# Kernel optimization log

Measured on AMD Instinct MI355X. Metric: run time of the kernel, lower is better.

## Reference

```python
import jax, jax.numpy as jnp
import numpy as np

B_IMG = 2
N_PROP = 2000
N_GT = 16
C_FEAT = 256
H_FEAT = 128
W_FEAT = 128
IMG = 1024.0
NUM_CLASSES = 2
BG_THRESH = 0.5          # fg==bg==0.5 -> BETWEEN_THRESHOLDS band is empty
BPI = 512                # batch_size_per_image
NUM_POS_MAX = int(BPI * 0.25)
ENC_W = (1.0, 1.0, 1.0, 1.0, 1.0)
SCALE = 1.0 / 8.0        # feature stride
POOL = 7
SR = 2                   # sampling_ratio
BETA = 1.0 / 9.0
HID = 1024


def _make_boxes(key, shape_prefix, img=IMG):
    kc, ks = jax.random.split(key)
    c = jax.random.uniform(kc, shape_prefix + (2,), minval=0.0, maxval=img)
    s = jax.random.uniform(ks, shape_prefix + (2,), minval=20.0, maxval=200.0)
    lo = jnp.clip(c - 0.5 * s, 0.0, img - 2.0)
    hi = jnp.clip(c + 0.5 * s, lo + 1.0, img)
    return jnp.concatenate([lo, hi], axis=-1)  # [.., x1,y1,x2,y2]


def setup_inputs():
    key = jax.random.key(0)
    ks = jax.random.split(key, 12)
    features = jax.random.normal(ks[0], (B_IMG, C_FEAT, H_FEAT, W_FEAT), dtype=jnp.float32)
    proposals = _make_boxes(ks[1], (B_IMG, N_PROP))
    gt_boxes = _make_boxes(ks[2], (B_IMG, N_GT))
    gt_labels = jax.random.randint(ks[3], (B_IMG, N_GT), 1, NUM_CLASSES, dtype=jnp.int32)
    ka, kb, kt = jax.random.split(ks[4], 3)
    a = jax.random.uniform(ka, (B_IMG, N_GT), minval=10.0, maxval=60.0)
    b = jax.random.uniform(kb, (B_IMG, N_GT), minval=5.0, maxval=30.0)
    th = jax.random.uniform(kt, (B_IMG, N_GT), minval=-np.pi / 2, maxval=np.pi / 2)
    exy = 0.5 * (gt_boxes[..., :2] + gt_boxes[..., 2:])
    gt_ellipses = jnp.stack([a, b, exy[..., 0], exy[..., 1], th], axis=-1)
    d_in = C_FEAT * POOL * POOL
    w1 = jax.random.normal(ks[5], (d_in, HID), dtype=jnp.float32) * 0.02
    b1 = jnp.zeros((HID,), jnp.float32)
    w2 = jax.random.normal(ks[6], (HID, HID), dtype=jnp.float32) * 0.02
    b2 = jnp.zeros((HID,), jnp.float32)
    wc = jax.random.normal(ks[7], (HID, NUM_CLASSES), dtype=jnp.float32) * 0.02
    bc = jnp.zeros((NUM_CLASSES,), jnp.float32)
    wr = jax.random.normal(ks[8], (HID, NUM_CLASSES * 6), dtype=jnp.float32) * 0.02
    br = jnp.zeros((NUM_CLASSES * 6,), jnp.float32)
    return dict(features=features, proposals=proposals, gt_boxes=gt_boxes,
                gt_labels=gt_labels, gt_ellipses=gt_ellipses,
                w1=w1, b1=b1, w2=w2, b2=b2, wc=wc, bc=bc, wr=wr, br=br)


def box_iou(b1, b2):  # [G,4], [P,4] -> [G,P]
    a1 = (b1[:, 2] - b1[:, 0]) * (b1[:, 3] - b1[:, 1])
    a2 = (b2[:, 2] - b2[:, 0]) * (b2[:, 3] - b2[:, 1])
    lt = jnp.maximum(b1[:, None, :2], b2[None, :, :2])
    rb = jnp.minimum(b1[:, None, 2:], b2[None, :, 2:])
    wh = jnp.clip(rb - lt, 0.0)
    inter = wh[..., 0] * wh[..., 1]
    return inter / (a1[:, None] + a2[None, :] - inter)


def encode_ellipses(ell, boxes):  # ell [..,5]=(a,b,cx,cy,theta), boxes [..,4] -> [..,6]
    a, b, ex, ey, th = (ell[..., i] for i in range(5))
    w = jnp.maximum(boxes[..., 2] - boxes[..., 0], 1.0)
    h = jnp.maximum(boxes[..., 3] - boxes[..., 1], 1.0)
    cx = 0.5 * (boxes[..., 0] + boxes[..., 2])
    cy = 0.5 * (boxes[..., 1] + boxes[..., 3])
    wx, wy, wa, wb, wt = ENC_W
    dx = wx * (ex - cx) / w
    dy = wy * (ey - cy) / h
    da = wa * jnp.log(jnp.maximum(2.0 * a, 1e-3) / w)
    db = wb * jnp.log(jnp.maximum(2.0 * b, 1e-3) / h)
    return jnp.stack([dx, dy, da, db, wt * jnp.sin(2.0 * th), wt * jnp.cos(2.0 * th)], axis=-1)


def roi_align(fmap, rois):  # [C,H,W], [R,4] -> [R,C,POOL,POOL]
    C, H, W = fmap.shape
    r = rois * SCALE
    x1, y1, x2, y2 = r[:, 0], r[:, 1], r[:, 2], r[:, 3]
    bw = jnp.maximum(x2 - x1, 1.0) / POOL
    bh = jnp.maximum(y2 - y1, 1.0) / POOL
    S = POOL * SR
    off = (jnp.arange(S, dtype=jnp.float32) + 0.5) / SR  # bin-unit sample offsets
    ys = jnp.clip(y1[:, None] + off[None, :] * bh[:, None], 0.0, H - 1.0)  # [R,S]
    xs = jnp.clip(x1[:, None] + off[None, :] * bw[:, None], 0.0, W - 1.0)
    y0 = jnp.clip(jnp.floor(ys), 0, H - 2).astype(jnp.int32)
    x0 = jnp.clip(jnp.floor(xs), 0, W - 2).astype(jnp.int32)
    ly = ys - y0
    lx = xs - x0
    Ya, Yb = y0[:, :, None], (y0 + 1)[:, :, None]  # [R,S,1]
    Xa, Xb = x0[:, None, :], (x0 + 1)[:, None, :]  # [R,1,S]
    v00 = fmap[:, Ya, Xa]; v01 = fmap[:, Ya, Xb]   # [C,R,S,S]
    v10 = fmap[:, Yb, Xa]; v11 = fmap[:, Yb, Xb]
    wy1 = ly[:, :, None]; wy0 = 1.0 - wy1
    wx1 = lx[:, None, :]; wx0 = 1.0 - wx1
    val = v00 * (wy0 * wx0) + v01 * (wy0 * wx1) + v10 * (wy1 * wx0) + v11 * (wy1 * wx1)
    R = rois.shape[0]
    pooled = val.reshape(C, R, POOL, SR, POOL, SR).mean(axis=(3, 5))
    return pooled.transpose(1, 0, 2, 3)


def reference(features, proposals, gt_boxes, gt_labels, gt_ellipses,
              w1, b1, w2, b2, wc, bc, wr, br):
    B = features.shape[0]
    # add_gt_proposals
    props = jnp.concatenate([proposals, gt_boxes], axis=1)            # [B,P,4]
    # assign_targets_to_proposals: IoU + Matcher (fg=bg=0.5)
    iou = jax.vmap(box_iou)(gt_boxes, props)                          # [B,G,P]
    matched_vals = iou.max(axis=1)
    matches = iou.argmax(axis=1)                                      # [B,P]
    lab = jnp.take_along_axis(gt_labels, matches, axis=1)
    lab = jnp.where(matched_vals < BG_THRESH, 0, lab)                 # background
    # BalancedPositiveNegativeSampler (deterministic, fixed-shape):
    # cap positives at NUM_POS_MAX by random rank, fill rest with random negatives
    rand = jax.random.uniform(jax.random.key(42), lab.shape)
    is_pos = lab > 0
    is_neg = lab == 0
    pos_s = jnp.where(is_pos, rand, -1e9)
    rank = jnp.argsort(jnp.argsort(-pos_s, axis=1), axis=1)
    capped = is_pos & (rank < NUM_POS_MAX)
    prio = jnp.where(capped, rand + 2.0, jnp.where(is_neg, rand, -1e9))
    _, idx = jax.lax.top_k(prio, BPI)                                 # [B,512]
    boxes = jnp.take_along_axis(props, idx[..., None], axis=1)        # [B,512,4]
    labels = jnp.take_along_axis(lab, idx, axis=1)                    # [B,512]
    m = jnp.take_along_axis(matches, idx, axis=1)
    ell = jnp.take_along_axis(gt_ellipses, m[..., None], axis=1)      # [B,512,5]
    targets = encode_ellipses(ell, boxes)                             # [B,512,6]
    # RoIAlign + TwoMLPHead + predictor
    pooled = jax.vmap(roi_align)(features, boxes)                     # [B,512,C,7,7]
    N = B * BPI
    x = pooled.reshape(N, -1)
    x = jax.nn.relu(x @ w1 + b1)
    x = jax.nn.relu(x @ w2 + b2)
    logits = x @ wc + bc                                              # [N,2]
    reg = (x @ wr + br).reshape(N, NUM_CLASSES, 6)
    # ellipse_rcnn_loss
    labels_f = labels.reshape(N)
    t = targets.reshape(N, 6)
    ce = -jnp.take_along_axis(jax.nn.log_softmax(logits, axis=-1), labels_f[:, None], axis=1).mean()
    pred = jnp.take_along_axis(reg, labels_f[:, None, None], axis=1)[:, 0]  # [N,6]
    d = jnp.abs(pred - t)
    sl1 = jnp.where(d < BETA, 0.5 * d * d / BETA, d - 0.5 * BETA)
    reg_loss = jnp.sum(sl1 * (labels_f > 0)[:, None].astype(sl1.dtype)) / N
    return jnp.stack([ce, reg_loss])
```

## Files before the change

kernel.cpp:

```cpp
#include <hip/hip_runtime.h>
#include <hip/hip_bf16.h>
#include <math.h>

#define B_IMG   2
#define N_PROP  2000
#define N_GT    16
#define NPROPS  2016
#define C_FEAT  256
#define H_FEAT  128
#define W_FEAT  128
#define HWF     (H_FEAT*W_FEAT)
#define POOL    7
#define BPI     512
#define NPOSMAX 128
#define NSEL    (B_IMG*BPI)
#define K1      (C_FEAT*POOL*POOL)
#define K1P     12800
#define HID     1024
#define NHEAD   14
#define SPLITK1 8
#define G1_KC   1600

typedef short bf16x8f __attribute__((ext_vector_type(8)));
typedef float f32x4f  __attribute__((ext_vector_type(4)));
typedef short short4v __attribute__((ext_vector_type(4)));

__device__ __forceinline__ void threefry2x32(unsigned k0, unsigned k1,
                                             unsigned& x0, unsigned& x1) {
  unsigned ks[3] = {k0, k1, k0 ^ k1 ^ 0x1BD11BDAu};
  const int R0[4] = {13, 15, 26, 6};
  const int R1[4] = {17, 29, 16, 24};
  x0 += ks[0]; x1 += ks[1];
#pragma unroll
  for (int g = 0; g < 5; g++) {
    const int* rot = (g & 1) ? R1 : R0;
#pragma unroll
    for (int r = 0; r < 4; r++) {
      x0 += x1;
      x1 = (x1 << rot[r]) | (x1 >> (32 - rot[r]));
      x1 ^= x0;
    }
    x0 += ks[(g + 1) % 3];
    x1 += ks[(g + 2) % 3] + (unsigned)(g + 1);
  }
}

#define PRE_SAMPLE   2
#define PRE_TRANS    (PRE_SAMPLE + 2048)
#define PRE_CAST1    (PRE_TRANS + 3136)
#define PRE_CAST0    (PRE_CAST1 + 256)
#define PRE_TOTAL    (PRE_CAST0 + 512)

__global__ __launch_bounds__(256) void k_pre(const float* __restrict__ proposals,
                                             const float* __restrict__ gt_boxes,
                                             const int* __restrict__ gt_labels,
                                             const float* __restrict__ features,
                                             const float* __restrict__ w1,
                                             const float* __restrict__ w2,
                                             const float* __restrict__ gt_ell,
                                             __hip_bfloat16* __restrict__ featT,
                                             __hip_bfloat16* __restrict__ W1T,
                                             __hip_bfloat16* __restrict__ W2T,
                                             __hip_bfloat16* __restrict__ Xb,
                                             float* __restrict__ sel_boxes,
                                             int* __restrict__ sel_labels,
                                             float* __restrict__ targets) {
  __shared__ __align__(16) char smem[16640];
  int bid = blockIdx.x;
  int tid = threadIdx.x;
  if (bid < PRE_SAMPLE) {
    float* rs           = (float*)smem;
    unsigned char* mtl  = (unsigned char*)(smem + 8064);
    short* pos_i        = (short*)(smem + 10080);
    short* glist        = (short*)(smem + 10080);
    int*   Hs           = (int*)(smem + 14112);
    int*   curs         = (int*)(smem + 15140);
    float* gtb          = (float*)(smem + 16176);
    int*   gtl          = (int*)(smem + 16432);
    int*   cnt          = (int*)(smem + 16496);
    int b = bid;
    int base = b * NPROPS;
    if (tid == 0) *cnt = 0;
    if (tid < N_GT * 4) gtb[tid] = gt_boxes[b * N_GT * 4 + tid];
    if (tid < N_GT) gtl[tid] = gt_labels[b * N_GT + tid];
    __syncthreads();

    auto emitsel = [&](int slot, int i, int lab) {
      float p0, p1, p2, p3;
      if (i < N_PROP) {
        const float4 v = *(const float4*)(proposals + ((size_t)b * N_PROP + i) * 4);
        p0 = v.x; p1 = v.y; p2 = v.z; p3 = v.w;
      } else {
        const float* g = &gtb[(i - N_PROP) * 4];
        p0 = g[0]; p1 = g[1]; p2 = g[2]; p3 = g[3];
      }
      sel_boxes[slot * 4 + 0] = p0;
      sel_boxes[slot * 4 + 1] = p1;
      sel_boxes[slot * 4 + 2] = p2;
      sel_boxes[slot * 4 + 3] = p3;
      sel_labels[slot] = lab;
      int m = mtl[i] & 15;
      const float* e = gt_ell + ((size_t)b * N_GT + m) * 5;
      float ea = e[0], eb = e[1], ex = e[2], ey = e[3], eth = e[4];
      float w = fmaxf(p2 - p0, 1.0f), h = fmaxf(p3 - p1, 1.0f);
      float cx = 0.5f * (p0 + p2), cy = 0.5f * (p1 + p3);
      float* t = targets + (size_t)slot * 6;
      t[0] = (ex - cx) / w;
      t[1] = (ey - cy) / h;
      t[2] = logf(fmaxf(2.0f * ea, 0.001f) / w);
      t[3] = logf(fmaxf(2.0f * eb, 0.001f) / h);
      t[4] = sinf(2.0f * eth);
      t[5] = cosf(2.0f * eth);
    };

    for (int i = tid; i < NPROPS; i += 256) {
      unsigned x0 = 0u, x1 = (unsigned)(base + i);
      threefry2x32(0u, 42u, x0, x1);
      unsigned bits = x0 ^ x1;
      float r = __uint_as_float((bits >> 9) | 0x3F800000u) - 1.0f;
      rs[i] = r;
      float p0, p1, p2, p3;
      if (i < N_PROP) {
        const float4 v = *(const float4*)(proposals + ((size_t)b * N_PROP + i) * 4);
        p0 = v.x; p1 = v.y; p2 = v.z; p3 = v.w;
      } else {
        const float* g = &gtb[(i - N_PROP) * 4];
        p0 = g[0]; p1 = g[1]; p2 = g[2]; p3 = g[3];
      }
      float a2 = (p2 - p0) * (p3 - p1);
      float best = -1.0f; int bg = 0;
#pragma unroll
      for (int g = 0; g < N_GT; g++) {
        float g0 = gtb[g*4], g1 = gtb[g*4+1], g2 = gtb[g*4+2], g3 = gtb[g*4+3];
        float a1 = (g2 - g0) * (g3 - g1);
        float wx = fmaxf(fminf(g2, p2) - fmaxf(g0, p0), 0.0f);
        float wy = fmaxf(fminf(g3, p3) - fmaxf(g1, p1), 0.0f);
        float inter = wx * wy;
        float iou = inter / (a1 + a2 - inter);
        if (iou > best) { best = iou; bg = g; }
      }
      int lab = (best < 0.5f) ? 0 : gtl[bg];
      mtl[i] = (unsigned char)(bg | (lab ? 16 : 0));
      if (lab > 0) {
        int s = atomicAdd(cnt, 1);
        pos_i[s] = (short)i;
      }
    }
    __syncthreads();
    int P = *cnt;
    int Pp = (P < NPOSMAX) ? P : NPOSMAX;
    for (int s = tid; s < P; s += 256) {
      int i = pos_i[s]; float ri = rs[i];
      int ch = 0;
      for (int j = 0; j < P; j++) {
        int ij = pos_i[j]; float rj = rs[ij];
        ch += (rj > ri || (rj == ri && ij < i)) ? 1 : 0;
      }
      if (ch < NPOSMAX) {
        int m16 = mtl[i] & 15;
        int lab = gtl[m16];
        emitsel(b * BPI + ch, i, lab);
      }
    }
    __syncthreads();
    for (int idx = tid; idx < 257; idx += 256) Hs[idx] = 0;
    curs[tid] = 0;
    __syncthreads();
    for (int i = tid; i < NPROPS; i += 256)
      if (!(mtl[i] & 16)) {
        int bin = (int)(rs[i] * 256.0f); if (bin > 255) bin = 255;
        atomicAdd(&Hs[bin], 1);
      }
    __syncthreads();
    for (int off = 1; off < 256; off <<= 1) {
      int v = Hs[tid] + ((tid + off <= 256) ? Hs[tid + off] : 0);
      __syncthreads();
      Hs[tid] = v;
      __syncthreads();
    }
    for (int i = tid; i < NPROPS; i += 256)
      if (!(mtl[i] & 16)) {
        int bin = (int)(rs[i] * 256.0f); if (bin > 255) bin = 255;
        int o = atomicAdd(&curs[bin], 1);
        glist[Hs[bin + 1] + o] = (short)i;
      }
    __syncthreads();
    for (int i = tid; i < NPROPS; i += 256)
      if (!(mtl[i] & 16)) {
        int bin = (int)(rs[i] * 256.0f); if (bin > 255) bin = 255;
        int bbase = Hs[bin + 1];
        int cntb = Hs[bin] - bbase;
        float ri = rs[i];
        int wr = 0;
        for (int t = 0; t < cntb; t++) {
          int j = glist[bbase + t];
          if (j != i) {
            float rj = rs[j];
            wr += (rj > ri || (rj == ri && j < i)) ? 1 : 0;
          }
        }
        int slot = Pp + bbase + wr;
        if (slot < BPI) emitsel(b * BPI + slot, i, 0);
      }
  } else if (bid < PRE_TRANS) {
    float (*tile)[65] = (float(*)[65])smem;
    int t = bid - PRE_SAMPLE;
    int b = t >> 10;
    int rem = t & 1023;
    int c0 = (rem >> 8) * 64;
    int s0 = (rem & 255) * 64;
    const float* src = features + (size_t)b * C_FEAT * HWF;
    __hip_bfloat16* dst = featT + (size_t)b * HWF * C_FEAT;
    int hw4 = (tid & 15) * 4, cr = tid >> 4;
#pragma unroll
    for (int p = 0; p < 4; p++) {
      int c = cr + p * 16;
      float4 v = *(const float4*)(src + (size_t)(c0 + c) * HWF + s0 + hw4);
      tile[hw4 + 0][c] = v.x; tile[hw4 + 1][c] = v.y;
      tile[hw4 + 2][c] = v.z; tile[hw4 + 3][c] = v.w;
    }
    __syncthreads();
    int c4 = (tid & 15) * 4, hr = tid >> 4;
#pragma unroll
    for (int p = 0; p < 4; p++) {
      int hw = hr + p * 16;
      __hip_bfloat16 o[4] = {__float2bfloat16(tile[hw][c4]), __float2bfloat16(tile[hw][c4+1]),
                             __float2bfloat16(tile[hw][c4+2]), __float2bfloat16(tile[hw][c4+3])};
      *(short4v*)(dst + (size_t)(s0 + hw) * C_FEAT + c0 + c4) = *(short4v*)o;
    }
  } else if (bid < PRE_CAST1) {
    float (*tile)[65] = (float(*)[65])smem;
    int t = bid - PRE_TRANS;
    int p = t >> 6;
    int rem = t & 63;
    int c0 = (rem & 3) * 64;
    int n0 = (rem >> 2) * 64;
    int n4 = (tid & 15) * 4, ig = tid >> 4;
#pragma unroll
    for (int i = ig; i < 64; i += 16) {
      float4 v = *(const float4*)(w1 + (size_t)((c0 + i) * 49 + p) * HID + n0 + n4);
      tile[i][n4] = v.x; tile[i][n4 + 1] = v.y;
      tile[i][n4 + 2] = v.z; tile[i][n4 + 3] = v.w;
    }
    __syncthreads();
    int c4 = (tid & 15) * 4;
#pragma unroll
    for (int i = ig; i < 64; i += 16) {
      __hip_bfloat16 o[4] = {__float2bfloat16(tile[c4][i]), __float2bfloat16(tile[c4 + 1][i]),
                             __float2bfloat16(tile[c4 + 2][i]), __float2bfloat16(tile[c4 + 3][i])};
      *(short4v*)(W1T + (size_t)(n0 + i) * K1P + p * 256 + c0 + c4) = *(short4v*)o;
    }
  } else if (bid < PRE_CAST0) {
    float (*tile)[65] = (float(*)[65])smem;
    int t = bid - PRE_CAST1;
    int c0 = (t & 15) * 64;
    int n0 = (t >> 4) * 64;
    int n4 = (tid & 15) * 4, ig = tid >> 4;
#pragma unroll
    for (int i = ig; i < 64; i += 16) {
      float4 v = *(const float4*)(w2 + (size_t)(c0 + i) * HID + n0 + n4);
      tile[i][n4] = v.x; tile[i][n4 + 1] = v.y;
      tile[i][n4 + 2] = v.z; tile[i][n4 + 3] = v.w;
    }
    __syncthreads();
    int c4 = (tid & 15) * 4;
#pragma unroll
    for (int i = ig; i < 64; i += 16) {
      __hip_bfloat16 o[4] = {__float2bfloat16(tile[c4][i]), __float2bfloat16(tile[c4 + 1][i]),
                             __float2bfloat16(tile[c4 + 2][i]), __float2bfloat16(tile[c4 + 3][i])};
      *(short4v*)(W2T + (size_t)(n0 + i) * HID + c0 + c4) = *(short4v*)o;
    }
  } else {
    int t = bid - PRE_CAST0;
    __hip_bfloat16* buf = (t >> 8) ? W1T : Xb;
    int tt = (t & 255) * 256 + tid;
    int row = tt >> 6;
    int col4 = (tt & 63) << 2;
    short4v z = {0, 0, 0, 0};
    *(short4v*)(buf + (size_t)row * K1P + K1 + col4) = z;
  }
}

__global__ __launch_bounds__(256) void k_roialign(const __hip_bfloat16* __restrict__ featT,
                                                  const float* __restrict__ sel_boxes,
                                                  __hip_bfloat16* __restrict__ X) {
  int n = blockIdx.x;
  int py = blockIdx.y;
  int t = threadIdx.x;
  int px = t >> 5;
  int lane32 = t & 31;
  int c = lane32 << 3;
  int b = n >> 9;
  const float* bx = sel_boxes + (size_t)n * 4;
  float x1 = bx[0] * 0.125f, y1 = bx[1] * 0.125f;
  float x2 = bx[2] * 0.125f, y2 = bx[3] * 0.125f;
  float bw = fmaxf(x2 - x1, 1.0f) / 7.0f;
  float bh = fmaxf(y2 - y1, 1.0f) / 7.0f;
  if (px >= 7) return;
  const __hip_bfloat16* base = featT + (size_t)b * HWF * C_FEAT;
  int y0A[2]; float lyA[2];
#pragma unroll
  for (int sy = 0; sy < 2; sy++) {
    float off = ((float)(py * 2 + sy) + 0.5f) * 0.5f;
    float ys = fminf(fmaxf(y1 + off * bh, 0.0f), 127.0f);
    int y0 = (int)fminf(fmaxf(floorf(ys), 0.0f), 126.0f);
    y0A[sy] = y0; lyA[sy] = ys - (float)y0;
  }
  float acc[8] = {};
#pragma unroll
  for (int sx = 0; sx < 2; sx++) {
    float off = ((float)(px * 2 + sx) + 0.5f) * 0.5f;
    float xs = fminf(fmaxf(x1 + off * bw, 0.0f), 127.0f);
    int x0 = (int)fminf(fmaxf(floorf(xs), 0.0f), 126.0f);
    float lx = xs - (float)x0;
#pragma unroll
    for (int sy = 0; sy < 2; sy++) {
      int y0 = y0A[sy]; float ly = lyA[sy];
      const __hip_bfloat16* p = base + ((size_t)(y0 * W_FEAT + x0)) * C_FEAT + c;
      bf16x8f s00 = *(const bf16x8f*)p;
      bf16x8f s01 = *(const bf16x8f*)(p + C_FEAT);
      bf16x8f s10 = *(const bf16x8f*)(p + W_FEAT * C_FEAT);
      bf16x8f s11 = *(const bf16x8f*)(p + W_FEAT * C_FEAT + C_FEAT);
      float w00 = (1.0f - ly) * (1.0f - lx), w01 = (1.0f - ly) * lx;
      float w10 = ly * (1.0f - lx), w11 = ly * lx;
#pragma unroll
      for (int q = 0; q < 8; q++) {
        float v00 = __uint_as_float(((unsigned)(unsigned short)s00[q]) << 16);
        float v01 = __uint_as_float(((unsigned)(unsigned short)s01[q]) << 16);
        float v10 = __uint_as_float(((unsigned)(unsigned short)s10[q]) << 16);
        float v11 = __uint_as_float(((unsigned)(unsigned short)s11[q]) << 16);
        acc[q] += v00 * w00 + v01 * w01 + v10 * w10 + v11 * w11;
      }
    }
  }
  __hip_bfloat16 o[8];
#pragma unroll
  for (int q = 0; q < 8; q++) o[q] = __float2bfloat16(acc[q] * 0.25f);
  *(bf16x8f*)&X[(size_t)n * K1P + (size_t)(py * 7 + px) * C_FEAT + c] = *(bf16x8f*)o;
}

__device__ __forceinline__ void gld_lds16(const __hip_bfloat16* g, __hip_bfloat16* l) {
  __builtin_amdgcn_global_load_lds(
      (const __attribute__((address_space(1))) void*)g,
      (__attribute__((address_space(3))) void*)l, 16, 0, 0);
}

__global__ __launch_bounds__(256) void k_gemm1s(const __hip_bfloat16* __restrict__ A,
                                                const __hip_bfloat16* __restrict__ BT,
                                                __hip_bfloat16* __restrict__ Pb) {
  __shared__ __align__(16) __hip_bfloat16 As[128 * 32];
  __shared__ __align__(16) __hip_bfloat16 Bs[128 * 32];
  int lin = blockIdx.x;
  int kz = lin & 7;
  int q  = lin >> 3;
  int n0 = (q & 7) * 128;
  int m0 = (q >> 3) * 128;
  int tid = threadIdx.x;
  int kbeg = kz * G1_KC;
  int srow = tid >> 2;
  int scs  = tid & 3;
  int sg   = scs ^ (srow & 3);
  int scol = sg << 3;
  int wave = tid >> 6, lane = tid & 63;
  int wm = (wave & 1) * 64, wn = (wave >> 1) * 64;
  int lm = lane & 15, quad = lane >> 4;
  int fco = ((quad ^ (lm & 3)) << 3);
  f32x4f acc[4][4] = {};
  for (int k0 = kbeg; k0 < kbeg + G1_KC; k0 += 32) {
    __syncthreads();
#pragma unroll
    for (int r0 = 0; r0 < 128; r0 += 64)
      gld_lds16(A + (size_t)(m0 + r0 + srow) * K1P + k0 + scol, &As[(r0 + srow) * 32 + scs * 8]);
#pragma unroll
    for (int r0 = 0; r0 < 128; r0 += 64)
      gld_lds16(BT + (size_t)(n0 + r0 + srow) * K1P + k0 + scol, &Bs[(r0 + srow) * 32 + scs * 8]);
    __syncthreads();
    bf16x8f af[4], bf[4];
#pragma unroll
    for (int i = 0; i < 4; i++)
      af[i] = *(const bf16x8f*)&As[(wm + i * 16 + lm) * 32 + fco];
#pragma unroll
    for (int j = 0; j < 4; j++)
      bf[j] = *(const bf16x8f*)&Bs[(wn + j * 16 + lm) * 32 + fco];
#pragma unroll
    for (int i = 0; i < 4; i++)
#pragma unroll
      for (int j = 0; j < 4; j++)
        acc[i][j] = __builtin_amdgcn_mfma_f32_16x16x32_bf16(af[i], bf[j], acc[i][j], 0, 0, 0);
  }
  int tileoff = ((m0 >> 7) * 8 + (n0 >> 7)) * 16384;
  __hip_bfloat16* dst = Pb + ((size_t)kz << 20) + tileoff + wave * 4096 + lane * 4;
#pragma unroll
  for (int i = 0; i < 4; i++)
#pragma unroll
    for (int j = 0; j < 4; j++) {
      __hip_bfloat16 o[4] = {__float2bfloat16(acc[i][j][0]), __float2bfloat16(acc[i][j][1]),
                             __float2bfloat16(acc[i][j][2]), __float2bfloat16(acc[i][j][3])};
      *(short4v*)(dst + (i * 4 + j) * 256) = *(short4v*)o;
    }
}

__global__ __launch_bounds__(256) void k_reduce16(const __hip_bfloat16* __restrict__ Pb,
                                                  const float* __restrict__ bias,
                                                  __hip_bfloat16* __restrict__ O) {
  int m4 = blockIdx.x >> 2;
  int n  = (blockIdx.x & 3) * 256 + threadIdx.x;
  int m0i = m4 >> 5, wavem = (m4 >> 4) & 1, i = (m4 >> 2) & 3, quad = m4 & 3;
  int n0i = n >> 7, wn_i = (n >> 6) & 1, j = (n >> 4) & 3, lm = n & 15;
  int wave = wavem + wn_i * 2;
  int elem = (m0i * 8 + n0i) * 16384 + wave * 4096 + (i * 4 + j) * 256 + (quad * 16 + lm) * 4;
  float s0 = 0.0f, s1 = 0.0f, s2 = 0.0f, s3 = 0.0f;
#pragma unroll
  for (int z = 0; z < SPLITK1; z++) {
    short4v v = *(const short4v*)(Pb + ((size_t)z << 20) + elem);
    s0 += __uint_as_float(((unsigned)(unsigned short)v[0]) << 16);
    s1 += __uint_as_float(((unsigned)(unsigned short)v[1]) << 16);
    s2 += __uint_as_float(((unsigned)(unsigned short)v[2]) << 16);
    s3 += __uint_as_float(((unsigned)(unsigned short)v[3]) << 16);
  }
  float bv = bias[n];
  int m = m4 * 4;
  O[(size_t)(m + 0) * HID + n] = __float2bfloat16(fmaxf(s0 + bv, 0.0f));
  O[(size_t)(m + 1) * HID + n] = __float2bfloat16(fmaxf(s1 + bv, 0.0f));
  O[(size_t)(m + 2) * HID + n] = __float2bfloat16(fmaxf(s2 + bv, 0.0f));
  O[(size_t)(m + 3) * HID + n] = __float2bfloat16(fmaxf(s3 + bv, 0.0f));
}

#define G2_NKT  16
#define G2_ABUF 8192
#define G2_BUFE 16384
#define H2P     129

__global__ __launch_bounds__(512, 1) void k_gemm2h(const __hip_bfloat16* __restrict__ A,
                                                   const __hip_bfloat16* __restrict__ BT,
                                                   const float* __restrict__ b2,
                                                   const float* __restrict__ wc,
                                                   const float* __restrict__ wr,
                                                   float* __restrict__ Ypart,
                                                   const float* __restrict__ bc,
                                                   const float* __restrict__ br,
                                                   const int* __restrict__ sel_labels,
                                                   const float* __restrict__ T,
                                                   float* __restrict__ out,
                                                   int* __restrict__ loss_cnt) {
  __shared__ __align__(16) char smem[3 * G2_BUFE * 2];
  __shared__ int lastf;
  __hip_bfloat16* slds = (__hip_bfloat16*)smem;
  float* h2 = (float*)smem;
  float* wh = (float*)(smem + 128 * H2P * 4);
  const int m0 = (blockIdx.x >> 3) * 128;
  const int nb = blockIdx.x & 7;
  const int n0 = nb * 128;
  const int tid = threadIdx.x;
  const int wave = tid >> 6, lane = tid & 63;
  const int wm = (wave & 1) * 64, wn = (wave >> 1) * 32;
  const int lm = lane & 15, quad = lane >> 4;

  f32x4f acc[4][2] = {};

  auto stage = [&](int kt, int sb) {
    const int kcol = kt * 64;
    __hip_bfloat16* lb = slds + sb * G2_BUFE;
#pragma unroll
    for (int u = 0; u < 2; ++u) {
      int idx = tid + u * 512;
      int r = idx >> 3, g = (idx & 7) ^ (r & 7);
      gld_lds16(A + (size_t)(m0 + r) * HID + kcol + g * 8, lb + idx * 8);
    }
#pragma unroll
    for (int u = 0; u < 2; ++u) {
      int idx = tid + u * 512;
      int r = idx >> 3, g = (idx & 7) ^ (r & 7);
      gld_lds16(BT + (size_t)(n0 + r) * HID + kcol + g * 8, lb + G2_ABUF + idx * 8);
    }
  };

  stage(0, 0);
  stage(1, 1);
  asm volatile("s_waitcnt vmcnt(4)" ::: "memory");
  __builtin_amdgcn_s_barrier();

  int buf = 0;
  for (int kt = 0; kt < G2_NKT; ++kt) {
    int sb = buf + 2; if (sb >= 3) sb -= 3;
    if (kt + 2 < G2_NKT) stage(kt + 2, sb);
    const __hip_bfloat16* Ab = slds + buf * G2_BUFE;
    const __hip_bfloat16* Bb = Ab + G2_ABUF;
    bf16x8f af[4][2], bf[2][2];
#pragma unroll
    for (int i = 0; i < 4; ++i)
#pragma unroll
      for (int s = 0; s < 2; ++s)
        af[i][s] = *(const bf16x8f*)(Ab + (wm + i * 16 + lm) * 64 +
                                     (((s << 2) + quad) ^ (lm & 7)) * 8);
#pragma unroll
    for (int j = 0; j < 2; ++j)
#pragma unroll
      for (int s = 0; s < 2; ++s)
        bf[j][s] = *(const bf16x8f*)(Bb + (wn + j * 16 + lm) * 64 +
                                     (((s << 2) + quad) ^ (lm & 7)) * 8);
    __builtin_amdgcn_s_setprio(1);
#pragma unroll
    for (int s = 0; s < 2; ++s)
#pragma unroll
      for (int i = 0; i < 4; ++i)
#pragma unroll
        for (int j = 0; j < 2; ++j)
          acc[i][j] = __builtin_amdgcn_mfma_f32_16x16x32_bf16(af[i][s], bf[j][s], acc[i][j], 0, 0, 0);
    __builtin_amdgcn_s_setprio(0);
    if (kt < G2_NKT - 1) {
      if (kt < G2_NKT - 2) asm volatile("s_waitcnt vmcnt(4)" ::: "memory");
      else                 asm volatile("s_waitcnt vmcnt(0)" ::: "memory");
      __builtin_amdgcn_s_barrier();
    }
    buf = (buf == 2) ? 0 : buf + 1;
  }
  __syncthreads();

  float bb[2];
#pragma unroll
  for (int j = 0; j < 2; ++j) bb[j] = b2[n0 + wn + j * 16 + lm];
#pragma unroll
  for (int i = 0; i < 4; ++i)
#pragma unroll
    for (int j = 0; j < 2; ++j) {
      int col = wn + j * 16 + lm;
#pragma unroll
      for (int r = 0; r < 4; ++r) {
        int row = wm + i * 16 + quad * 4 + r;
        h2[row * H2P + col] = fmaxf(acc[i][j][r] + bb[j], 0.0f);
      }
    }
  for (int idx = tid; idx < 128 * 14; idx += 512) {
    int nl = idx / 14, j = idx - nl * 14;
    wh[idx] = (j < 2) ? wc[(size_t)(n0 + nl) * 2 + j]
                      : wr[(size_t)(n0 + nl) * 12 + (j - 2)];
  }
  __syncthreads();
  {
    int rrow = tid & 127, jg = tid >> 7;
    int j0 = jg * 4, jn = (jg == 3) ? 2 : 4;
    float s[4] = {};
#pragma unroll 4
    for (int k = 0; k < 128; ++k) {
      float h = h2[rrow * H2P + k];
      const float* w = wh + k * 14 + j0;
#pragma unroll
      for (int j = 0; j < 4; ++j) s[j] += h * w[j];
    }
    float* yp = Ypart + ((size_t)nb * NSEL + m0 + rrow) * 16 + j0;
    for (int j = 0; j < jn; ++j) yp[j] = s[j];
  }
  __syncthreads();
  if (tid == 0) {
    __threadfence();
    int old = atomicAdd(loss_cnt, 1);
    lastf = ((old & 63) == 63) ? 1 : 0;
  }
  __syncthreads();
  if (!lastf) return;
  __threadfence();
  float* sc = (float*)smem;
  float* sr = sc + 512;
  float ce_s = 0.0f, rg_s = 0.0f;
#pragma unroll
  for (int half = 0; half < 2; ++half) {
    int n = tid + half * 512;
    float y[14];
#pragma unroll
    for (int j = 0; j < 14; ++j) y[j] = (j < 2) ? bc[j] : br[j - 2];
#pragma unroll
    for (int nb2 = 0; nb2 < 8; ++nb2) {
      const float* p = Ypart + ((size_t)nb2 * NSEL + n) * 16;
      float4 v0 = *(const float4*)(p + 0);
      float4 v1 = *(const float4*)(p + 4);
      float4 v2 = *(const float4*)(p + 8);
      float2 v3 = *(const float2*)(p + 12);
      y[0] += v0.x; y[1] += v0.y; y[2] += v0.z; y[3] += v0.w;
      y[4] += v1.x; y[5] += v1.y; y[6] += v1.z; y[7] += v1.w;
      y[8] += v2.x; y[9] += v2.y; y[10] += v2.z; y[11] += v2.w;
      y[12] += v3.x; y[13] += v3.y;
    }
    int lb = sel_labels[n];
    float mx = fmaxf(y[0], y[1]);
    float lse = mx + logf(expf(y[0] - mx) + expf(y[1] - mx));
    ce_s += lse - (lb ? y[1] : y[0]);
    if (lb > 0) {
      const float beta = 1.0f / 9.0f;
      const float* t = T + (size_t)n * 6;
#pragma unroll
      for (int j = 0; j < 6; j++) {
        float d = fabsf(y[2 + lb * 6 + j] - t[j]);
        rg_s += (d < beta) ? (0.5f * d * d / beta) : (d - 0.5f * beta);
      }
    }
  }
  sc[tid] = ce_s; sr[tid] = rg_s;
  __syncthreads();
  for (int sft = 256; sft > 0; sft >>= 1) {
    if (tid < sft) { sc[tid] += sc[tid + sft]; sr[tid] += sr[tid + sft]; }
    __syncthreads();
  }
  if (tid == 0) {
    out[0] = sc[0] * (1.0f / 1024.0f);
    out[1] = sr[0] * (1.0f / 1024.0f);
  }
}

extern "C" void kernel_launch(void* const* d_in, const int* in_sizes, int n_in,
                              void* d_out, int out_size, void* d_ws, size_t ws_size,
                              hipStream_t stream) {
  const float* features  = (const float*)d_in[0];
  const float* proposals = (const float*)d_in[1];
  const float* gt_boxes  = (const float*)d_in[2];
  const int*   gt_labels = (const int*)d_in[3];
  const float* gt_ell    = (const float*)d_in[4];
  const float* w1 = (const float*)d_in[5];
  const float* b1 = (const float*)d_in[6];
  const float* w2 = (const float*)d_in[7];
  const float* b2 = (const float*)d_in[8];
  const float* wc = (const float*)d_in[9];
  const float* bc = (const float*)d_in[10];
  const float* wr = (const float*)d_in[11];
  const float* br = (const float*)d_in[12];
  float* out = (float*)d_out;

  char* ws = (char*)d_ws;
  size_t off = 0;
  auto take = [&](size_t bytes) -> void* {
    void* p = ws + off;
    off = (off + bytes + 255) & ~(size_t)255;
    return p;
  };
  __hip_bfloat16* Pb = (__hip_bfloat16*)take((size_t)16 * (1 << 20) * 2);
  __hip_bfloat16* featT = Pb;
  __hip_bfloat16* Xb  = (__hip_bfloat16*)take((size_t)NSEL * K1P * 2);
  __hip_bfloat16* W1T = (__hip_bfloat16*)take((size_t)HID * K1P * 2);
  __hip_bfloat16* W2T = (__hip_bfloat16*)take((size_t)HID * HID * 2);
  __hip_bfloat16* H1b = (__hip_bfloat16*)take((size_t)NSEL * HID * 2);
  float* Ypart     = (float*)take((size_t)8 * NSEL * 16 * 4);
  float* sel_boxes = (float*)take((size_t)NSEL * 4 * 4);
  int*   sel_lab   = (int*)take((size_t)NSEL * 4);
  float* targets   = (float*)take((size_t)NSEL * 6 * 4);
  int*   loss_cnt  = (int*)take(256);

  k_pre<<<PRE_TOTAL, 256, 0, stream>>>(proposals, gt_boxes, gt_labels, features,
                                       w1, w2, gt_ell, featT, W1T, W2T, Xb,
                                       sel_boxes, sel_lab, targets);
  k_roialign<<<dim3(NSEL, POOL), 256, 0, stream>>>(featT, sel_boxes, Xb);

  k_gemm1s<<<512, 256, 0, stream>>>(Xb, W1T, Pb);
  k_reduce16<<<1024, 256, 0, stream>>>(Pb, b1, H1b);
  k_gemm2h<<<64, 512, 0, stream>>>(H1b, W2T, b2, wc, wr, Ypart,
                                   bc, br, sel_lab, targets, out, loss_cnt);
}
```

Baseline: 259.7 us.

## Move proposal selection ranking into a separate massively parallel kernel

The sampling blocks of k_pre now only compute IoU matches, labels and a priority key per proposal, writing them to global memory. A new k_select kernel ranks every proposal with one wavefront per proposal and a shuffle reduction, then emits the selected boxes, labels and ellipse targets. This replaces the serial histogram and bucket ranking that ran in just two blocks inside k_pre, which likely lengthened the tail of that kernel. In exchange it adds a kernel launch, extra global round trips, and O(N^2) rank comparisons spread across many blocks.

Result: faster. 240.4 us (-7.4%).

```diff
diff --git a/kernel.cpp b/kernel.cpp
--- a/kernel.cpp
+++ b/kernel.cpp
@@ -57,62 +57,28 @@
                                              const float* __restrict__ features,
                                              const float* __restrict__ w1,
                                              const float* __restrict__ w2,
-                                             const float* __restrict__ gt_ell,
+                                             float* __restrict__ prio,
+                                             int* __restrict__ plab,
+                                             int* __restrict__ matches,
                                              __hip_bfloat16* __restrict__ featT,
                                              __hip_bfloat16* __restrict__ W1T,
                                              __hip_bfloat16* __restrict__ W2T,
-                                             __hip_bfloat16* __restrict__ Xb,
-                                             float* __restrict__ sel_boxes,
-                                             int* __restrict__ sel_labels,
-                                             float* __restrict__ targets) {
+                                             __hip_bfloat16* __restrict__ Xb) {
   __shared__ __align__(16) char smem[16640];
   int bid = blockIdx.x;
   int tid = threadIdx.x;
   if (bid < PRE_SAMPLE) {
-    float* rs           = (float*)smem;
-    unsigned char* mtl  = (unsigned char*)(smem + 8064);
-    short* pos_i        = (short*)(smem + 10080);
-    short* glist        = (short*)(smem + 10080);
-    int*   Hs           = (int*)(smem + 14112);
-    int*   curs         = (int*)(smem + 15140);
-    float* gtb          = (float*)(smem + 16176);
-    int*   gtl          = (int*)(smem + 16432);
-    int*   cnt          = (int*)(smem + 16496);
+    float* rs    = (float*)smem;
+    short* pos_i = (short*)(smem + 8064);
+    float* gtb   = (float*)(smem + 12096);
+    int*   gtl   = (int*)(smem + 12352);
+    int*   cnt   = (int*)(smem + 12416);
     int b = bid;
     int base = b * NPROPS;
     if (tid == 0) *cnt = 0;
     if (tid < N_GT * 4) gtb[tid] = gt_boxes[b * N_GT * 4 + tid];
     if (tid < N_GT) gtl[tid] = gt_labels[b * N_GT + tid];
     __syncthreads();
-
-    auto emitsel = [&](int slot, int i, int lab) {
-      float p0, p1, p2, p3;
-      if (i < N_PROP) {
-        const float4 v = *(const float4*)(proposals + ((size_t)b * N_PROP + i) * 4);
-        p0 = v.x; p1 = v.y; p2 = v.z; p3 = v.w;
-      } else {
-        const float* g = &gtb[(i - N_PROP) * 4];
-        p0 = g[0]; p1 = g[1]; p2 = g[2]; p3 = g[3];
-      }
-      sel_boxes[slot * 4 + 0] = p0;
-      sel_boxes[slot * 4 + 1] = p1;
-      sel_boxes[slot * 4 + 2] = p2;
-      sel_boxes[slot * 4 + 3] = p3;
-      sel_labels[slot] = lab;
-      int m = mtl[i] & 15;
-      const float* e = gt_ell + ((size_t)b * N_GT + m) * 5;
-      float ea = e[0], eb = e[1], ex = e[2], ey = e[3], eth = e[4];
-      float w = fmaxf(p2 - p0, 1.0f), h = fmaxf(p3 - p1, 1.0f);
-      float cx = 0.5f * (p0 + p2), cy = 0.5f * (p1 + p3);
-      float* t = targets + (size_t)slot * 6;
-      t[0] = (ex - cx) / w;
-      t[1] = (ey - cy) / h;
-      t[2] = logf(fmaxf(2.0f * ea, 0.001f) / w);
-      t[3] = logf(fmaxf(2.0f * eb, 0.001f) / h);
-      t[4] = sinf(2.0f * eth);
-      t[5] = cosf(2.0f * eth);
-    };
-
     for (int i = tid; i < NPROPS; i += 256) {
       unsigned x0 = 0u, x1 = (unsigned)(base + i);
       threefry2x32(0u, 42u, x0, x1);
@@ -139,8 +105,9 @@
         float iou = inter / (a1 + a2 - inter);
         if (iou > best) { best = iou; bg = g; }
       }
+      matches[base + i] = bg;
       int lab = (best < 0.5f) ? 0 : gtl[bg];
-      mtl[i] = (unsigned char)(bg | (lab ? 16 : 0));
+      plab[base + i] = lab;
       if (lab > 0) {
         int s = atomicAdd(cnt, 1);
         pos_i[s] = (short)i;
@@ -148,7 +115,7 @@
     }
     __syncthreads();
     int P = *cnt;
-    int Pp = (P < NPOSMAX) ? P : NPOSMAX;
+    int ii[8]; float nv[8]; int nloc = 0;
     for (int s = tid; s < P; s += 256) {
       int i = pos_i[s]; float ri = rs[i];
       int ch = 0;
@@ -156,52 +123,13 @@
         int ij = pos_i[j]; float rj = rs[ij];
         ch += (rj > ri || (rj == ri && ij < i)) ? 1 : 0;
       }
-      if (ch < NPOSMAX) {
-        int m16 = mtl[i] & 15;
-        int lab = gtl[m16];
-        emitsel(b * BPI + ch, i, lab);
-      }
-    }
-    __syncthreads();
-    for (int idx = tid; idx < 257; idx += 256) Hs[idx] = 0;
-    curs[tid] = 0;
-    __syncthreads();
-    for (int i = tid; i < NPROPS; i += 256)
-      if (!(mtl[i] & 16)) {
-        int bin = (int)(rs[i] * 256.0f); if (bin > 255) bin = 255;
-        atomicAdd(&Hs[bin], 1);
-      }
-    __syncthreads();
-    for (int off = 1; off < 256; off <<= 1) {
-      int v = Hs[tid] + ((tid + off <= 256) ? Hs[tid + off] : 0);
-      __syncthreads();
-      Hs[tid] = v;
-      __syncthreads();
-    }
-    for (int i = tid; i < NPROPS; i += 256)
-      if (!(mtl[i] & 16)) {
-        int bin = (int)(rs[i] * 256.0f); if (bin > 255) bin = 255;
-        int o = atomicAdd(&curs[bin], 1);
-        glist[Hs[bin + 1] + o] = (short)i;
-      }
-    __syncthreads();
-    for (int i = tid; i < NPROPS; i += 256)
-      if (!(mtl[i] & 16)) {
-        int bin = (int)(rs[i] * 256.0f); if (bin > 255) bin = 255;
-        int bbase = Hs[bin + 1];
-        int cntb = Hs[bin] - bbase;
-        float ri = rs[i];
-        int wr = 0;
-        for (int t = 0; t < cntb; t++) {
-          int j = glist[bbase + t];
-          if (j != i) {
-            float rj = rs[j];
-            wr += (rj > ri || (rj == ri && j < i)) ? 1 : 0;
-          }
-        }
-        int slot = Pp + bbase + wr;
-        if (slot < BPI) emitsel(b * BPI + slot, i, 0);
-      }
+      ii[nloc] = i;
+      nv[nloc++] = (ch < NPOSMAX) ? (ri + 2.0f) : -1000000000.0f;
+    }
+    __syncthreads();
+    for (int k2 = 0; k2 < nloc; k2++) rs[ii[k2]] = nv[k2];
+    __syncthreads();
+    for (int i = tid; i < NPROPS; i += 256) prio[base + i] = rs[i];
   } else if (bid < PRE_TRANS) {
     float (*tile)[65] = (float(*)[65])smem;
     int t = bid - PRE_SAMPLE;
@@ -279,6 +207,55 @@
     short4v z = {0, 0, 0, 0};
     *(short4v*)(buf + (size_t)row * K1P + K1 + col4) = z;
   }
+}
+
+__global__ __launch_bounds__(256) void k_select(const float* __restrict__ prio,
+    const float* __restrict__ proposals, const float* __restrict__ gt_boxes,
+    const int* __restrict__ matches, const int* __restrict__ plab,
+    const float* __restrict__ gt_ell,
+    float* __restrict__ sel_boxes, int* __restrict__ sel_labels,
+    float* __restrict__ targets) {
+  int tid = threadIdx.x;
+  int wave = tid >> 6, lane = tid & 63;
+  int b = blockIdx.y;
+  int base = b * NPROPS;
+  int i = blockIdx.x * 4 + wave;
+  float pi = prio[base + i];
+  int rank = 0;
+  for (int j = lane; j < NPROPS; j += 64) {
+    float pj = prio[base + j];
+    rank += (pj > pi || (pj == pi && j < i)) ? 1 : 0;
+  }
+#pragma unroll
+  for (int off = 32; off > 0; off >>= 1) rank += __shfl_down(rank, off);
+  if (lane != 0 || rank >= BPI) return;
+  int slot = b * BPI + rank;
+  float p0, p1, p2, p3;
+  if (i < N_PROP) {
+    const float* p = proposals + ((size_t)b * N_PROP + i) * 4;
+    p0 = p[0]; p1 = p[1]; p2 = p[2]; p3 = p[3];
+  } else {
+    const float* p = gt_boxes + ((size_t)b * N_GT + (i - N_PROP)) * 4;
+    p0 = p[0]; p1 = p[1]; p2 = p[2]; p3 = p[3];
+  }
+  sel_boxes[slot * 4 + 0] = p0;
+  sel_boxes[slot * 4 + 1] = p1;
+  sel_boxes[slot * 4 + 2] = p2;
+  sel_boxes[slot * 4 + 3] = p3;
+  int lb = plab[base + i];
+  sel_labels[slot] = lb;
+  int m = matches[base + i];
+  const float* e = gt_ell + ((size_t)b * N_GT + m) * 5;
+  float ea = e[0], eb = e[1], ex = e[2], ey = e[3], eth = e[4];
+  float w = fmaxf(p2 - p0, 1.0f), h = fmaxf(p3 - p1, 1.0f);
+  float cx = 0.5f * (p0 + p2), cy = 0.5f * (p1 + p3);
+  float* t = targets + (size_t)slot * 6;
+  t[0] = (ex - cx) / w;
+  t[1] = (ey - cy) / h;
+  t[2] = logf(fmaxf(2.0f * ea, 0.001f) / w);
+  t[3] = logf(fmaxf(2.0f * eb, 0.001f) / h);
+  t[4] = sinf(2.0f * eth);
+  t[5] = cosf(2.0f * eth);
 }
 
 __global__ __launch_bounds__(256) void k_roialign(const __hip_bfloat16* __restrict__ featT,
@@ -639,14 +616,20 @@
   __hip_bfloat16* W2T = (__hip_bfloat16*)take((size_t)HID * HID * 2);
   __hip_bfloat16* H1b = (__hip_bfloat16*)take((size_t)NSEL * HID * 2);
   float* Ypart     = (float*)take((size_t)8 * NSEL * 16 * 4);
+  int*   matches   = (int*)take((size_t)B_IMG * NPROPS * 4);
+  int*   plab      = (int*)take((size_t)B_IMG * NPROPS * 4);
+  float* prio      = (float*)take((size_t)B_IMG * NPROPS * 4);
   float* sel_boxes = (float*)take((size_t)NSEL * 4 * 4);
   int*   sel_lab   = (int*)take((size_t)NSEL * 4);
   float* targets   = (float*)take((size_t)NSEL * 6 * 4);
   int*   loss_cnt  = (int*)take(256);
 
   k_pre<<<PRE_TOTAL, 256, 0, stream>>>(proposals, gt_boxes, gt_labels, features,
-                                       w1, w2, gt_ell, featT, W1T, W2T, Xb,
-                                       sel_boxes, sel_lab, targets);
+                                       w1, w2, prio, plab, matches,
+                                       featT, W1T, W2T, Xb);
+  k_select<<<dim3(NPROPS / 4, B_IMG), 256, 0, stream>>>(prio, proposals, gt_boxes,
+                                                        matches, plab, gt_ell,
+                                                        sel_boxes, sel_lab, targets);
   k_roialign<<<dim3(NSEL, POOL), 256, 0, stream>>>(featT, sel_boxes, Xb);
 
   k_gemm1s<<<512, 256, 0, stream>>>(Xb, W1T, Pb);
```
